# Kernel optimization log

Hardware: AMD Instinct MI355X
Metric: run time of the kernel (lower is better)

## Reference

```python
import jax, jax.numpy as jnp
import numpy as np

B, L, D_MODEL, H, D_K, D_V = 64, 52, 4096, 32, 128, 128
NEW_C = D_MODEL // H  # per-head input channel after the (faithful) raw reshape


def setup_inputs() -> dict:
    key = jax.random.key(0)
    ks = jax.random.split(key, 12)
    s = 0.02
    return {
        "Q": jax.random.normal(ks[0], (B, L, D_MODEL), jnp.float32),
        "K": jax.random.normal(ks[1], (B, L, D_MODEL), jnp.float32),
        "V": jax.random.normal(ks[2], (B, L, D_MODEL), jnp.float32),
        "Wq": jax.random.normal(ks[3], (H, NEW_C, D_K), jnp.float32) * s,
        "bq": jnp.zeros((H, D_K), jnp.float32),
        "Wk": jax.random.normal(ks[4], (H, NEW_C, D_K), jnp.float32) * s,
        "bk": jnp.zeros((H, D_K), jnp.float32),
        "Wv": jax.random.normal(ks[5], (H, NEW_C, D_V), jnp.float32) * s,
        "bv": jnp.zeros((H, D_V), jnp.float32),
        "Wo": jax.random.normal(ks[6], (H * D_V, D_MODEL), jnp.float32) * s,
        "bo": jnp.zeros((D_MODEL,), jnp.float32),
    }


def reference(Q, K, V, Wq, bq, Wk, bk, Wv, bv, Wo, bo):
    # Faithful to source: raw reshape (B, L, D) -> (B, H, L, D/H), NOT a channel split.
    def split(x):
        return x.reshape(B, H, L, NEW_C)

    q = jnp.einsum('bhlc,hck->bhlk', split(Q), Wq) + bq[None, :, None, :]  # (B,H,L,D_K)
    k = jnp.einsum('bhlc,hck->bhlk', split(K), Wk) + bk[None, :, None, :]
    v = jnp.einsum('bhlc,hcv->bhlv', split(V), Wv) + bv[None, :, None, :]

    scores = jnp.einsum('bhqk,bhmk->bhqm', q, k) / jnp.sqrt(jnp.asarray(D_K, q.dtype))
    # causal mask: keep j <= i, else -inf (matches the numpy masking loop)
    causal = jnp.tril(jnp.ones((L, L), bool))
    scores = jnp.where(causal[None, None], scores, -jnp.inf)
    attn = jax.nn.softmax(scores, axis=-1)
    o = jnp.einsum('bhqm,bhmv->bhqv', attn, v)  # (B,H,L,D_V)
    o = o.transpose(0, 2, 1, 3).reshape(B, L, H * D_V)  # concat heads on last axis
    # Dropout(0.1) is identity at inference.
    return o @ Wo + bo
```

## Files before the change

### kernel.cpp

```cpp
#include <hip/hip_runtime.h>
#include <hip/hip_bf16.h>

#define B_SZ   64
#define L_SZ   52
#define DMODEL 4096
#define H_SZ   32
#define C_SZ   128
#define DK     128

#define GM 3328
#define GN 4096
#define GK 4096

typedef __bf16 bf16x8 __attribute__((ext_vector_type(8)));
typedef float  f32x4  __attribute__((ext_vector_type(4)));

__device__ __forceinline__ void gload_lds16(const void* g, void* l) {
  __builtin_amdgcn_global_load_lds(
      (__attribute__((address_space(1))) void*)(void*)g,
      (__attribute__((address_space(3))) void*)l, 16, 0, 0);
}

__device__ __forceinline__ unsigned short bfbits(float x) {
  union { __hip_bfloat16 h; unsigned short u; } c;
  c.h = __float2bfloat16(x);
  return c.u;
}

__global__ __launch_bounds__(256) void wo_transpose_kernel(
    const float* __restrict__ Wo, __hip_bfloat16* __restrict__ WoT) {
  __shared__ float tile[64][65];
  const int nt = blockIdx.x, mt = blockIdx.y;
  const int t = threadIdx.x;
  const int r  = t >> 4;
  const int c4 = (t & 15) << 2;
#pragma unroll
  for (int p = 0; p < 4; ++p) {
    const int rr = r + p * 16;
    const float4 v = *(const float4*)(Wo + (size_t)(mt * 64 + rr) * 4096 + nt * 64 + c4);
    tile[rr][c4 + 0] = v.x; tile[rr][c4 + 1] = v.y;
    tile[rr][c4 + 2] = v.z; tile[rr][c4 + 3] = v.w;
  }
  __syncthreads();
#pragma unroll
  for (int p = 0; p < 4; ++p) {
    const int rr = r + p * 16;
    union { __hip_bfloat16 h[4]; ushort4 u; } o4;
#pragma unroll
    for (int e = 0; e < 4; ++e) o4.h[e] = __float2bfloat16(tile[c4 + e][rr]);
    *(ushort4*)(WoT + (size_t)(nt * 64 + rr) * 4096 + mt * 64 + c4) = o4.u;
  }
}

__global__ __launch_bounds__(256) void w3_transpose_kernel(
    const float* __restrict__ Wq, const float* __restrict__ Wk,
    const float* __restrict__ Wv, __hip_bfloat16* __restrict__ WqT,
    __hip_bfloat16* __restrict__ WkT, __hip_bfloat16* __restrict__ WvT) {
  __shared__ float tile[64][65];
  const int bz = blockIdx.z;
  const float* in = (bz < 32 ? Wq : (bz < 64 ? Wk : Wv)) + (size_t)(bz & 31) * 16384;
  __hip_bfloat16* out = (bz < 32 ? WqT : (bz < 64 ? WkT : WvT)) + (size_t)(bz & 31) * 16384;
  const int nt = blockIdx.x, mt = blockIdx.y;
  const int t = threadIdx.x;
  const int r  = t >> 4;
  const int c4 = (t & 15) << 2;
#pragma unroll
  for (int p = 0; p < 4; ++p) {
    const int rr = r + p * 16;
    const float4 v = *(const float4*)(in + (size_t)(mt * 64 + rr) * 128 + nt * 64 + c4);
    tile[rr][c4 + 0] = v.x; tile[rr][c4 + 1] = v.y;
    tile[rr][c4 + 2] = v.z; tile[rr][c4 + 3] = v.w;
  }
  __syncthreads();
#pragma unroll
  for (int p = 0; p < 4; ++p) {
    const int rr = r + p * 16;
    union { __hip_bfloat16 h[4]; ushort4 u; } o4;
#pragma unroll
    for (int e = 0; e < 4; ++e) o4.h[e] = __float2bfloat16(tile[c4 + e][rr]);
    *(ushort4*)(out + (size_t)(nt * 64 + rr) * 128 + mt * 64 + c4) = o4.u;
  }
}

__device__ __forceinline__ void proj_lds(
    const __hip_bfloat16* __restrict__ xs, const __hip_bfloat16* __restrict__ WT,
    const float* __restrict__ bias, __hip_bfloat16* __restrict__ out,
    int n0, int r16, int kq) {
  f32x4 acc[4][2] = {};
  bf16x8 bfrag[2][4];
#pragma unroll
  for (int nt = 0; nt < 2; ++nt)
#pragma unroll
    for (int kk = 0; kk < 4; ++kk)
      bfrag[nt][kk] = *(const bf16x8*)(WT + (n0 + nt * 16 + r16) * 128 + kk * 32 + kq * 8);
#pragma unroll
  for (int kk = 0; kk < 4; ++kk) {
    bf16x8 a[4];
#pragma unroll
    for (int mt = 0; mt < 4; ++mt) {
      const int row = mt * 16 + r16;
      const int rowc = row < 52 ? row : 51;
      a[mt] = *(const bf16x8*)(xs + rowc * 136 + kk * 32 + kq * 8);
    }
#pragma unroll
    for (int mt = 0; mt < 4; ++mt)
#pragma unroll
      for (int nt = 0; nt < 2; ++nt)
        acc[mt][nt] = __builtin_amdgcn_mfma_f32_16x16x32_bf16(a[mt], bfrag[nt][kk], acc[mt][nt], 0, 0, 0);
  }
#pragma unroll
  for (int nt = 0; nt < 2; ++nt) {
    const int col = n0 + nt * 16 + r16;
    const float bv = bias[col];
#pragma unroll
    for (int mt = 0; mt < 4; ++mt) {
      const int m0 = mt * 16 + kq * 4;
      if (m0 < 52) {
#pragma unroll
        for (int i = 0; i < 4; ++i)
          if (m0 + i < 52)
            out[(m0 + i) * 136 + col] = __float2bfloat16(acc[mt][nt][i] + bv);
      }
    }
  }
}

__device__ __forceinline__ uint2 shfl64(uint2 v, int lane) {
  uint2 r;
  r.x = (unsigned)__shfl((int)v.x, lane);
  r.y = (unsigned)__shfl((int)v.y, lane);
  return r;
}

__global__ __launch_bounds__(256, 3) void attn_kernel(
    const float* __restrict__ Qin, const float* __restrict__ Kin,
    const float* __restrict__ Vin,
    const __hip_bfloat16* __restrict__ WqT, const float* __restrict__ bq,
    const __hip_bfloat16* __restrict__ WkT, const float* __restrict__ bk,
    const __hip_bfloat16* __restrict__ WvT, const float* __restrict__ bv,
    __hip_bfloat16* __restrict__ Oc) {
  __shared__ __align__(16) char lds[42432];
  __hip_bfloat16* r0 = (__hip_bfloat16*)(lds);
  __hip_bfloat16* r1 = (__hip_bfloat16*)(lds + 14144);
  __hip_bfloat16* r2 = (__hip_bfloat16*)(lds + 28288);
  float*          s_sh = (float*)(lds + 14144);
  __hip_bfloat16* p_sh = r0;

  const int h = blockIdx.x, bb = blockIdx.y;
  const int t = threadIdx.x;
  const int w = t >> 6, lane = t & 63;
  const int r16 = lane & 15, kq = lane >> 4;
  const size_t xoff = (size_t)bb * (L_SZ * DMODEL) + (size_t)h * (L_SZ * C_SZ);
  const int n0 = w * 32;

  {
    const float* xp[3] = {Qin + xoff, Kin + xoff, Vin + xoff};
    __hip_bfloat16* xd[3] = {r0, r1, r2};
#pragma unroll
    for (int tz = 0; tz < 3; ++tz) {
      const float* X = xp[tz];
      __hip_bfloat16* xs = xd[tz];
      for (int idx = t; idx < 52 * 32; idx += 256) {
        const int row = idx >> 5, c4 = (idx & 31) << 2;
        const float4 v = *(const float4*)(X + row * 128 + c4);
        union { __hip_bfloat16 h[4]; ushort4 u; } o4;
        o4.h[0] = __float2bfloat16(v.x); o4.h[1] = __float2bfloat16(v.y);
        o4.h[2] = __float2bfloat16(v.z); o4.h[3] = __float2bfloat16(v.w);
        *(ushort4*)(xs + row * 136 + c4) = o4.u;
      }
    }
  }
  __syncthreads();

  uint2 vb[4][2];
  {
    f32x4 acc[4][2] = {};
    bf16x8 bfrag[2][4];
    const __hip_bfloat16* WT = WvT + (size_t)h * 16384;
#pragma unroll
    for (int nt = 0; nt < 2; ++nt)
#pragma unroll
      for (int kk = 0; kk < 4; ++kk)
        bfrag[nt][kk] = *(const bf16x8*)(WT + (n0 + nt * 16 + r16) * 128 + kk * 32 + kq * 8);
#pragma unroll
    for (int kk = 0; kk < 4; ++kk) {
      bf16x8 a[4];
#pragma unroll
      for (int mt = 0; mt < 4; ++mt) {
        const int row = mt * 16 + r16;
        const int rowc = row < 52 ? row : 51;
        a[mt] = *(const bf16x8*)(r2 + rowc * 136 + kk * 32 + kq * 8);
      }
#pragma unroll
      for (int mt = 0; mt < 4; ++mt)
#pragma unroll
        for (int nt = 0; nt < 2; ++nt)
          acc[mt][nt] = __builtin_amdgcn_mfma_f32_16x16x32_bf16(a[mt], bfrag[nt][kk], acc[mt][nt], 0, 0, 0);
    }
#pragma unroll
    for (int nt = 0; nt < 2; ++nt) {
      const float bvv = bv[h * 128 + n0 + nt * 16 + r16];
#pragma unroll
      for (int mt = 0; mt < 4; ++mt) {
        vb[mt][nt].x = (unsigned)bfbits(acc[mt][nt][0] + bvv) |
                       ((unsigned)bfbits(acc[mt][nt][1] + bvv) << 16);
        vb[mt][nt].y = (unsigned)bfbits(acc[mt][nt][2] + bvv) |
                       ((unsigned)bfbits(acc[mt][nt][3] + bvv) << 16);
      }
    }
  }
  __syncthreads();

  proj_lds(r0, WqT + (size_t)h * 16384, bq + h * 128, r2, n0, r16, kq);
  __syncthreads();

  proj_lds(r1, WkT + (size_t)h * 16384, bk + h * 128, r0, n0, r16, kq);
  __syncthreads();

  {
    const int nq = w * 16;
    f32x4 sacc[4] = {};
#pragma unroll
    for (int kk = 0; kk < 4; ++kk) {
      const int krow = nq + r16;
      const int krc = krow < 52 ? krow : 51;
      const bf16x8 bf_ = *(const bf16x8*)(r0 + krc * 136 + kk * 32 + kq * 8);
#pragma unroll
      for (int mt = 0; mt < 4; ++mt) {
        const int qrow = mt * 16 + r16;
        const int qrc = qrow < 52 ? qrow : 51;
        const bf16x8 a = *(const bf16x8*)(r2 + qrc * 136 + kk * 32 + kq * 8);
        sacc[mt] = __builtin_amdgcn_mfma_f32_16x16x32_bf16(a, bf_, sacc[mt], 0, 0, 0);
      }
    }
    const float scale = 0.08838834764831845f;
#pragma unroll
    for (int mt = 0; mt < 4; ++mt)
#pragma unroll
      for (int i = 0; i < 4; ++i) {
        const int row = mt * 16 + kq * 4 + i;
        if (row < 52) s_sh[row * 68 + nq + r16] = sacc[mt][i] * scale;
      }
  }
  __syncthreads();

  {
    const int r = t >> 2, qd = t & 3;
    if (r < 52) {
      float v[16];
      float mx = -3e38f;
#pragma unroll
      for (int j4 = 0; j4 < 4; ++j4) {
        const f32x4 s4 = *(const f32x4*)(s_sh + r * 68 + qd * 16 + j4 * 4);
#pragma unroll
        for (int e = 0; e < 4; ++e) {
          const int col = qd * 16 + j4 * 4 + e;
          const float val = (col <= r) ? s4[e] : -3e38f;
          v[j4 * 4 + e] = val;
          mx = fmaxf(mx, val);
        }
      }
      mx = fmaxf(mx, __shfl_xor(mx, 1));
      mx = fmaxf(mx, __shfl_xor(mx, 2));
      float ex[16];
      float sum = 0.f;
#pragma unroll
      for (int j = 0; j < 16; ++j) {
        const int col = qd * 16 + j;
        const float e = (col <= r) ? __expf(v[j] - mx) : 0.f;
        ex[j] = e; sum += e;
      }
      sum += __shfl_xor(sum, 1);
      sum += __shfl_xor(sum, 2);
      const float inv = 1.0f / sum;
      union { __hip_bfloat16 h[8]; uint4 q; } p0, p1;
#pragma unroll
      for (int j = 0; j < 8; ++j) {
        p0.h[j] = __float2bfloat16(ex[j] * inv);
        p1.h[j] = __float2bfloat16(ex[8 + j] * inv);
      }
      *(uint4*)(p_sh + r * 72 + qd * 16)     = p0.q;
      *(uint4*)(p_sh + r * 72 + qd * 16 + 8) = p1.q;
    }
  }
  __syncthreads();

  {
    const int half = (kq >> 1) & 1;
    const int src0 = ((kq & 1) << 5) + r16;
    const int src1 = src0 + 16;
    f32x4 oacc[4][2] = {};
#pragma unroll
    for (int kk = 0; kk < 2; ++kk) {
      bf16x8 bfr[2];
#pragma unroll
      for (int nt = 0; nt < 2; ++nt) {
        const uint2 a0 = shfl64(vb[2 * kk + 0][nt], src0);
        const uint2 a1 = shfl64(vb[2 * kk + 1][nt], src0);
        const uint2 b0 = shfl64(vb[2 * kk + 0][nt], src1);
        const uint2 b1 = shfl64(vb[2 * kk + 1][nt], src1);
        union { unsigned u[4]; bf16x8 v; } asm_;
        asm_.u[0] = half ? a1.x : a0.x;
        asm_.u[1] = half ? a1.y : a0.y;
        asm_.u[2] = half ? b1.x : b0.x;
        asm_.u[3] = half ? b1.y : b0.y;
        bfr[nt] = asm_.v;
      }
#pragma unroll
      for (int mt = 0; mt < 4; ++mt) {
        const int prow = mt * 16 + r16;
        const int prc = prow < 52 ? prow : 51;
        const bf16x8 a = *(const bf16x8*)(p_sh + prc * 72 + kk * 32 + kq * 8);
#pragma unroll
        for (int nt = 0; nt < 2; ++nt)
          oacc[mt][nt] = __builtin_amdgcn_mfma_f32_16x16x32_bf16(a, bfr[nt], oacc[mt][nt], 0, 0, 0);
      }
    }
    const size_t obase = (size_t)bb * 52 * 4096 + (size_t)h * 128;
#pragma unroll
    for (int nt = 0; nt < 2; ++nt) {
      const int col = n0 + nt * 16 + r16;
#pragma unroll
      for (int mt = 0; mt < 4; ++mt) {
        const int row0 = mt * 16 + kq * 4;
#pragma unroll
        for (int i = 0; i < 4; ++i) {
          const int row = row0 + i;
          if (row < 52)
            Oc[obase + (size_t)row * 4096 + col] = __float2bfloat16(oacc[mt][nt][i]);
        }
      }
    }
  }
}

#define STAGE(GBASE, REGOFF, KT, KS, WB) do {                                  \
    const __hip_bfloat16* s_ = (GBASE) + (size_t)(KT) * 64 + (KS) * 32;        \
    char* d_ = (WB) + (REGOFF) + ((KS) ? 16384 : 0) + t * 16;                  \
    gload_lds16(s_, d_);                                                       \
    gload_lds16(s_ + (size_t)128 * GK, d_ + 8192);                             \
  } while (0)

#define MFMA16(MQ, BF)                                                         \
  __builtin_amdgcn_sched_barrier(0);                                           \
  __builtin_amdgcn_s_setprio(1);                                               \
  _Pragma("unroll")                                                            \
  for (int mf = 0; mf < 4; ++mf)                                               \
    _Pragma("unroll")                                                          \
    for (int nf = 0; nf < 4; ++nf)                                             \
      acc[(MQ) * 4 + mf][nf] = __builtin_amdgcn_mfma_f32_16x16x32_bf16(        \
          af[mf], BF[nf], acc[(MQ) * 4 + mf][nf], 0, 0, 0);                    \
  __builtin_amdgcn_s_setprio(0)

#define READ_AF(KS, MQ)                                                        \
  _Pragma("unroll")                                                            \
  for (int mf = 0; mf < 4; ++mf)                                               \
    af[mf] = *(const bf16x8*)(rb + (KS) * 16384 + (MQ) * 4096 + aB0 + mf * 1024)

#define READ_BF(BF, KS)                                                        \
  _Pragma("unroll")                                                            \
  for (int nf = 0; nf < 4; ++nf)                                               \
    BF[nf] = *(const bf16x8*)(rb + 32768 + (KS) * 16384 + bB0 + nf * 1024)

__global__ __launch_bounds__(512, 2) void out_gemm_kernel(
    const __hip_bfloat16* __restrict__ A, const __hip_bfloat16* __restrict__ Bt,
    const float* __restrict__ bias, float* __restrict__ C) {
  __shared__ __align__(16) char lds[131072];

  int bid = blockIdx.x;
  bid = (bid & 7) * 26 + (bid >> 3);
  const int tm = bid >> 4;
  const int tn = bid & 15;

  const int t = threadIdx.x;
  const int w = t >> 6, lane = t & 63;
  const int wm = w >> 2, wn = w & 3;
  const int r16 = lane & 15, kq = lane >> 4;

  const int srow = t >> 2;
  const int sgslot = (t & 3) ^ ((srow >> 1) & 3);
  const __hip_bfloat16* gA0 = A  + (size_t)(tm * 256 + srow) * GK + sgslot * 8;
  const __hip_bfloat16* gB0 = Bt + (size_t)(tn * 256 + srow) * GK + sgslot * 8;

  const int slotr = kq ^ ((r16 >> 1) & 3);
  const int aB0 = (wm * 128 + r16) * 64 + slotr * 16;
  const int bB0 = (wn * 64 + r16) * 64 + slotr * 16;

  f32x4 acc[8][4] = {};
  bf16x8 bf0[4], bf1[4];

  STAGE(gA0, 0,     0, 0, lds);
  STAGE(gA0, 0,     0, 1, lds);
  STAGE(gB0, 32768, 0, 0, lds);
  STAGE(gB0, 32768, 0, 1, lds);
  STAGE(gB0, 32768, 1, 0, lds + 65536);
  STAGE(gA0, 0,     1, 0, lds + 65536);
  STAGE(gB0, 32768, 1, 1, lds + 65536);
  asm volatile("s_waitcnt vmcnt(6)" ::: "memory");
  __builtin_amdgcn_s_barrier();

#pragma unroll 1
  for (int kt = 0; kt < 64; ++kt) {
    char* rb = lds + ((kt & 1) << 16);
    char* ob = lds + (((kt + 1) & 1) << 16);
    const int s1 = kt + 1 < 64 ? kt + 1 : 63;
    const int s2 = kt + 2 < 64 ? kt + 2 : 63;

    {
      bf16x8 af[4];
      READ_AF(0, 0);
      READ_BF(bf0, 0);
      STAGE(gA0, 0, s1, 1, ob);
      __builtin_amdgcn_s_barrier();
      asm volatile("s_waitcnt lgkmcnt(0)" ::: "memory");
      MFMA16(0, bf0);
      __builtin_amdgcn_s_barrier();
    }
    {
      bf16x8 af[4];
      READ_AF(0, 1);
      STAGE(gB0, 32768, s2, 0, rb);
      __builtin_amdgcn_s_barrier();
      asm volatile("s_waitcnt lgkmcnt(0)" ::: "memory");
      MFMA16(1, bf0);
      __builtin_amdgcn_s_barrier();
    }
    {
      bf16x8 af[4];
      READ_AF(1, 0);
      READ_BF(bf1, 1);
      STAGE(gA0, 0, s2, 0, rb);
      __builtin_amdgcn_s_barrier();
      asm volatile("s_waitcnt lgkmcnt(0)" ::: "memory");
      MFMA16(0, bf1);
      __builtin_amdgcn_s_barrier();
    }
    {
      bf16x8 af[4];
      READ_AF(1, 1);
      STAGE(gB0, 32768, s2, 1, rb);
      __builtin_amdgcn_s_barrier();
      asm volatile("s_waitcnt lgkmcnt(0)" ::: "memory");
      MFMA16(1, bf1);
      asm volatile("s_waitcnt vmcnt(6)" ::: "memory");
      __builtin_amdgcn_s_barrier();
    }
  }
  asm volatile("s_waitcnt vmcnt(0) lgkmcnt(0)" ::: "memory");

  const int row0 = tm * 256 + wm * 128 + kq * 4;
  const int col0 = tn * 256 + wn * 64 + r16;
#pragma unroll
  for (int nf = 0; nf < 4; ++nf) {
    const int col = col0 + nf * 16;
    const float bv = bias[col];
#pragma unroll
    for (int mf = 0; mf < 8; ++mf) {
      const int row = row0 + mf * 16;
#pragma unroll
      for (int i = 0; i < 4; ++i)
        C[(size_t)(row + i) * GN + col] = acc[mf][nf][i] + bv;
    }
  }
}

extern "C" void kernel_launch(void* const* d_in, const int* in_sizes, int n_in,
                              void* d_out, int out_size, void* d_ws, size_t ws_size,
                              hipStream_t stream) {
  const float* Q  = (const float*)d_in[0];
  const float* K  = (const float*)d_in[1];
  const float* V  = (const float*)d_in[2];
  const float* Wq = (const float*)d_in[3];
  const float* bq = (const float*)d_in[4];
  const float* Wk = (const float*)d_in[5];
  const float* bk = (const float*)d_in[6];
  const float* Wv = (const float*)d_in[7];
  const float* bv = (const float*)d_in[8];
  const float* Wo = (const float*)d_in[9];
  const float* bo = (const float*)d_in[10];
  float* out = (float*)d_out;

  char* wsb = (char*)d_ws;
  __hip_bfloat16* WoT = (__hip_bfloat16*)wsb;
  __hip_bfloat16* Oc  = (__hip_bfloat16*)(wsb + (size_t)GN * GK * 2);
  __hip_bfloat16* WqT = (__hip_bfloat16*)(wsb + (size_t)GN * GK * 2 + (size_t)GM * GN * 2);
  __hip_bfloat16* WkT = WqT + (size_t)H_SZ * C_SZ * DK;
  __hip_bfloat16* WvT = WkT + (size_t)H_SZ * C_SZ * DK;

  w3_transpose_kernel<<<dim3(2, 2, 96), 256, 0, stream>>>(Wq, Wk, Wv, WqT, WkT, WvT);
  wo_transpose_kernel<<<dim3(64, 64), 256, 0, stream>>>(Wo, WoT);
  attn_kernel<<<dim3(H_SZ, B_SZ), 256, 0, stream>>>(Q, K, V, WqT, bq, WkT, bk, WvT, bv, Oc);
  out_gemm_kernel<<<dim3(13 * 16), 512, 0, stream>>>(Oc, WoT, bo, out);
}
```

Before: 207.3 us.

## Merge Wo transpose into attention launch and unroll GEMM k-loop by two

The separate Wo transpose/convert kernel becomes extra blocks (ids 2048 and up) appended to the attention kernel's 1D grid. This removes one launch and lets the transpose overlap with attention work. The output GEMM main loop is also unrolled by two with fixed double-buffer pointers, dropping the per-iteration buffer address arithmetic. The trade-offs are larger code size and transpose blocks that reserve the attention kernel's LDS allocation.

```diff
diff --git a/kernel.cpp b/kernel.cpp
--- a/kernel.cpp
+++ b/kernel.cpp
@@ -25,31 +25,6 @@
   union { __hip_bfloat16 h; unsigned short u; } c;
   c.h = __float2bfloat16(x);
   return c.u;
-}
-
-__global__ __launch_bounds__(256) void wo_transpose_kernel(
-    const float* __restrict__ Wo, __hip_bfloat16* __restrict__ WoT) {
-  __shared__ float tile[64][65];
-  const int nt = blockIdx.x, mt = blockIdx.y;
-  const int t = threadIdx.x;
-  const int r  = t >> 4;
-  const int c4 = (t & 15) << 2;
-#pragma unroll
-  for (int p = 0; p < 4; ++p) {
-    const int rr = r + p * 16;
-    const float4 v = *(const float4*)(Wo + (size_t)(mt * 64 + rr) * 4096 + nt * 64 + c4);
-    tile[rr][c4 + 0] = v.x; tile[rr][c4 + 1] = v.y;
-    tile[rr][c4 + 2] = v.z; tile[rr][c4 + 3] = v.w;
-  }
-  __syncthreads();
-#pragma unroll
-  for (int p = 0; p < 4; ++p) {
-    const int rr = r + p * 16;
-    union { __hip_bfloat16 h[4]; ushort4 u; } o4;
-#pragma unroll
-    for (int e = 0; e < 4; ++e) o4.h[e] = __float2bfloat16(tile[c4 + e][rr]);
-    *(ushort4*)(WoT + (size_t)(nt * 64 + rr) * 4096 + mt * 64 + c4) = o4.u;
-  }
 }
 
 __global__ __launch_bounds__(256) void w3_transpose_kernel(
@@ -132,23 +107,52 @@
   return r;
 }
 
-__global__ __launch_bounds__(256, 3) void attn_kernel(
+__global__ __launch_bounds__(256, 3) void attn_fused_kernel(
     const float* __restrict__ Qin, const float* __restrict__ Kin,
     const float* __restrict__ Vin,
     const __hip_bfloat16* __restrict__ WqT, const float* __restrict__ bq,
     const __hip_bfloat16* __restrict__ WkT, const float* __restrict__ bk,
     const __hip_bfloat16* __restrict__ WvT, const float* __restrict__ bv,
-    __hip_bfloat16* __restrict__ Oc) {
+    __hip_bfloat16* __restrict__ Oc,
+    const float* __restrict__ Wo, __hip_bfloat16* __restrict__ WoT) {
   __shared__ __align__(16) char lds[42432];
+  const int gid = blockIdx.x;
+  const int t = threadIdx.x;
+
+  if (gid >= 2048) {
+    float* tile = (float*)lds;
+    const int bid2 = gid - 2048;
+    const int nt = bid2 & 63, mt = bid2 >> 6;
+    const int r  = t >> 4;
+    const int c4 = (t & 15) << 2;
+#pragma unroll
+    for (int p = 0; p < 4; ++p) {
+      const int rr = r + p * 16;
+      const float4 v = *(const float4*)(Wo + (size_t)(mt * 64 + rr) * 4096 + nt * 64 + c4);
+      tile[rr * 65 + c4 + 0] = v.x; tile[rr * 65 + c4 + 1] = v.y;
+      tile[rr * 65 + c4 + 2] = v.z; tile[rr * 65 + c4 + 3] = v.w;
+    }
+    __syncthreads();
+#pragma unroll
+    for (int p = 0; p < 4; ++p) {
+      const int rr = r + p * 16;
+      union { __hip_bfloat16 h[4]; ushort4 u; } o4;
+#pragma unroll
+      for (int e = 0; e < 4; ++e) o4.h[e] = __float2bfloat16(tile[(c4 + e) * 65 + rr]);
+      *(ushort4*)(WoT + (size_t)(nt * 64 + rr) * 4096 + mt * 64 + c4) = o4.u;
+    }
+    return;
+  }
+
   __hip_bfloat16* r0 = (__hip_bfloat16*)(lds);
   __hip_bfloat16* r1 = (__hip_bfloat16*)(lds + 14144);
   __hip_bfloat16* r2 = (__hip_bfloat16*)(lds + 28288);
   float*          s_sh = (float*)(lds + 14144);
   __hip_bfloat16* p_sh = r0;
 
-  const int h = blockIdx.x, bb = blockIdx.y;
-  const int t = threadIdx.x;
-  const int w = t >> 6, lane = t & 63;
+  const int h = gid & 31, bb = gid >> 5;
+  const int lane = t & 63;
+  const int w = t >> 6;
   const int r16 = lane & 15, kq = lane >> 4;
   const size_t xoff = (size_t)bb * (L_SZ * DMODEL) + (size_t)h * (L_SZ * C_SZ);
   const int n0 = w * 32;
@@ -352,15 +356,59 @@
           af[mf], BF[nf], acc[(MQ) * 4 + mf][nf], 0, 0, 0);                    \
   __builtin_amdgcn_s_setprio(0)
 
-#define READ_AF(KS, MQ)                                                        \
+#define READ_AF(RB, KS, MQ)                                                    \
   _Pragma("unroll")                                                            \
   for (int mf = 0; mf < 4; ++mf)                                               \
-    af[mf] = *(const bf16x8*)(rb + (KS) * 16384 + (MQ) * 4096 + aB0 + mf * 1024)
-
-#define READ_BF(BF, KS)                                                        \
+    af[mf] = *(const bf16x8*)((RB) + (KS) * 16384 + (MQ) * 4096 + aB0 + mf * 1024)
+
+#define READ_BF(RB, BF, KS)                                                    \
   _Pragma("unroll")                                                            \
   for (int nf = 0; nf < 4; ++nf)                                               \
-    BF[nf] = *(const bf16x8*)(rb + 32768 + (KS) * 16384 + bB0 + nf * 1024)
+    BF[nf] = *(const bf16x8*)((RB) + 32768 + (KS) * 16384 + bB0 + nf * 1024)
+
+#define KTILE_BODY(KT, RB, OB) do {                                            \
+    const int s1 = (KT) + 1 < 64 ? (KT) + 1 : 63;                              \
+    const int s2 = (KT) + 2 < 64 ? (KT) + 2 : 63;                              \
+    {                                                                          \
+      bf16x8 af[4];                                                            \
+      READ_AF(RB, 0, 0);                                                       \
+      READ_BF(RB, bf0, 0);                                                     \
+      STAGE(gA0, 0, s1, 1, OB);                                                \
+      __builtin_amdgcn_s_barrier();                                            \
+      asm volatile("s_waitcnt lgkmcnt(0)" ::: "memory");                       \
+      MFMA16(0, bf0);                                                          \
+      __builtin_amdgcn_s_barrier();                                            \
+    }                                                                          \
+    {                                                                          \
+      bf16x8 af[4];                                                            \
+      READ_AF(RB, 0, 1);                                                       \
+      STAGE(gB0, 32768, s2, 0, RB);                                            \
+      __builtin_amdgcn_s_barrier();                                            \
+      asm volatile("s_waitcnt lgkmcnt(0)" ::: "memory");                       \
+      MFMA16(1, bf0);                                                          \
+      __builtin_amdgcn_s_barrier();                                            \
+    }                                                                          \
+    {                                                                          \
+      bf16x8 af[4];                                                            \
+      READ_AF(RB, 1, 0);                                                       \
+      READ_BF(RB, bf1, 1);                                                     \
+      STAGE(gA0, 0, s2, 0, RB);                                                \
+      __builtin_amdgcn_s_barrier();                                            \
+      asm volatile("s_waitcnt lgkmcnt(0)" ::: "memory");                       \
+      MFMA16(0, bf1);                                                          \
+      __builtin_amdgcn_s_barrier();                                            \
+    }                                                                          \
+    {                                                                          \
+      bf16x8 af[4];                                                            \
+      READ_AF(RB, 1, 1);                                                       \
+      STAGE(gB0, 32768, s2, 1, RB);                                            \
+      __builtin_amdgcn_s_barrier();                                            \
+      asm volatile("s_waitcnt lgkmcnt(0)" ::: "memory");                       \
+      MFMA16(1, bf1);                                                          \
+      asm volatile("s_waitcnt vmcnt(6)" ::: "memory");                         \
+      __builtin_amdgcn_s_barrier();                                            \
+    }                                                                          \
+  } while (0)
 
 __global__ __launch_bounds__(512, 2) void out_gemm_kernel(
     const __hip_bfloat16* __restrict__ A, const __hip_bfloat16* __restrict__ Bt,
@@ -389,62 +437,24 @@
   f32x4 acc[8][4] = {};
   bf16x8 bf0[4], bf1[4];
 
-  STAGE(gA0, 0,     0, 0, lds);
-  STAGE(gA0, 0,     0, 1, lds);
-  STAGE(gB0, 32768, 0, 0, lds);
-  STAGE(gB0, 32768, 0, 1, lds);
-  STAGE(gB0, 32768, 1, 0, lds + 65536);
-  STAGE(gA0, 0,     1, 0, lds + 65536);
-  STAGE(gB0, 32768, 1, 1, lds + 65536);
+  char* const buf0 = lds;
+  char* const buf1 = lds + 65536;
+
+  STAGE(gA0, 0,     0, 0, buf0);
+  STAGE(gA0, 0,     0, 1, buf0);
+  STAGE(gB0, 32768, 0, 0, buf0);
+  STAGE(gB0, 32768, 0, 1, buf0);
+  STAGE(gB0, 32768, 1, 0, buf1);
+  STAGE(gA0, 0,     1, 0, buf1);
+  STAGE(gB0, 32768, 1, 1, buf1);
   asm volatile("s_waitcnt vmcnt(6)" ::: "memory");
   __builtin_amdgcn_s_barrier();
 
 #pragma unroll 1
-  for (int kt = 0; kt < 64; ++kt) {
-    char* rb = lds + ((kt & 1) << 16);
-    char* ob = lds + (((kt + 1) & 1) << 16);
-    const int s1 = kt + 1 < 64 ? kt + 1 : 63;
-    const int s2 = kt + 2 < 64 ? kt + 2 : 63;
-
-    {
-      bf16x8 af[4];
-      READ_AF(0, 0);
-      READ_BF(bf0, 0);
-      STAGE(gA0, 0, s1, 1, ob);
-      __builtin_amdgcn_s_barrier();
-      asm volatile("s_waitcnt lgkmcnt(0)" ::: "memory");
-      MFMA16(0, bf0);
-      __builtin_amdgcn_s_barrier();
-    }
-    {
-      bf16x8 af[4];
-      READ_AF(0, 1);
-      STAGE(gB0, 32768, s2, 0, rb);
-      __builtin_amdgcn_s_barrier();
-      asm volatile("s_waitcnt lgkmcnt(0)" ::: "memory");
-      MFMA16(1, bf0);
-      __builtin_amdgcn_s_barrier();
-    }
-    {
-      bf16x8 af[4];
-      READ_AF(1, 0);
-      READ_BF(bf1, 1);
-      STAGE(gA0, 0, s2, 0, rb);
-      __builtin_amdgcn_s_barrier();
-      asm volatile("s_waitcnt lgkmcnt(0)" ::: "memory");
-      MFMA16(0, bf1);
-      __builtin_amdgcn_s_barrier();
-    }
-    {
-      bf16x8 af[4];
-      READ_AF(1, 1);
-      STAGE(gB0, 32768, s2, 1, rb);
-      __builtin_amdgcn_s_barrier();
-      asm volatile("s_waitcnt lgkmcnt(0)" ::: "memory");
-      MFMA16(1, bf1);
-      asm volatile("s_waitcnt vmcnt(6)" ::: "memory");
-      __builtin_amdgcn_s_barrier();
-    }
+  for (int kt2 = 0; kt2 < 32; ++kt2) {
+    const int kt = kt2 * 2;
+    KTILE_BODY(kt,     buf0, buf1);
+    KTILE_BODY(kt + 1, buf1, buf0);
   }
   asm volatile("s_waitcnt vmcnt(0) lgkmcnt(0)" ::: "memory");
 
@@ -488,7 +498,7 @@
   __hip_bfloat16* WvT = WkT + (size_t)H_SZ * C_SZ * DK;
 
   w3_transpose_kernel<<<dim3(2, 2, 96), 256, 0, stream>>>(Wq, Wk, Wv, WqT, WkT, WvT);
-  wo_transpose_kernel<<<dim3(64, 64), 256, 0, stream>>>(Wo, WoT);
-  attn_kernel<<<dim3(H_SZ, B_SZ), 256, 0, stream>>>(Q, K, V, WqT, bq, WkT, bk, WvT, bv, Oc);
+  attn_fused_kernel<<<dim3(2048 + 4096), 256, 0, stream>>>(
+      Q, K, V, WqT, bq, WkT, bk, WvT, bv, Oc, Wo, WoT);
   out_gemm_kernel<<<dim3(13 * 16), 512, 0, stream>>>(Oc, WoT, bo, out);
 }
```

Result: faster. 192.4 us (-7.2%).
